# Kernel optimization log

Hardware: AMD Instinct MI355X
Metric: run time of the kernel (lower is better)

The kernel has to match this reference:

```python
import jax, jax.numpy as jnp
import numpy as np

J = 128
H = W = 1024
D = 2
NUM_CLS = 15
DEFAULT_SIGMA = 4096.0
TOPK = 0.95
LOSS_WEIGHT = 1.0
EPS = 1e-7


def setup_inputs() -> dict:
    key = jax.random.key(0)
    k1, k2, k3, k4 = jax.random.split(key, 4)
    mu = jax.random.uniform(k1, (J, 2), minval=0.0, maxval=float(H), dtype=jnp.float32)
    A = jax.random.normal(k2, (J, 2, 2), dtype=jnp.float32) * 8.0
    sigma = A @ A.transpose(0, 2, 1) + 100.0 * jnp.eye(2, dtype=jnp.float32)  # SPD covariances
    label = jax.random.randint(k3, (J,), 0, NUM_CLS)
    image = jax.random.normal(k4, (3, H, W), dtype=jnp.float32)
    pos_thres = jnp.full((16,), 0.3, jnp.float32)
    neg_thres = jnp.full((16,), 0.05, jnp.float32)
    return dict(mu=mu, sigma=sigma, label=label, image=image,
                pos_thres=pos_thres, neg_thres=neg_thres)


def _resize_bilinear_ac(x, Ho, Wo):
    # bilinear upsample with align_corners=True (matches F.interpolate)
    h, w = x.shape
    ry = jnp.arange(Ho, dtype=jnp.float32) * (h - 1) / (Ho - 1)
    rx = jnp.arange(Wo, dtype=jnp.float32) * (w - 1) / (Wo - 1)
    y0 = jnp.floor(ry).astype(jnp.int32); y1 = jnp.minimum(y0 + 1, h - 1); wy = ry - y0
    x0 = jnp.floor(rx).astype(jnp.int32); x1 = jnp.minimum(x0 + 1, w - 1); wx = rx - x0
    top = x[y0][:, x0] * (1 - wx)[None] + x[y0][:, x1] * wx[None]
    bot = x[y1][:, x0] * (1 - wx)[None] + x[y1][:, x1] * wx[None]
    return top * (1 - wy)[:, None] + bot * wy[:, None]


def _forward(mu, sigma, label, image, pos_thres, neg_thres):
    h, w = H // D, W // D
    # grid exactly like torch.linspace(0, h, h) + meshgrid(indexing='xy')
    x = jnp.linspace(0.0, h, h)
    y = jnp.linspace(0.0, w, w)
    X, Y = jnp.meshgrid(x, y, indexing='xy')  # [h, w] (h == w)
    mm = jnp.round(jax.lax.stop_gradient(mu) / D)  # [J, 2]

    # 'gaussian-orientation': keep eigenvectors, rescale eigenvalues to default area
    Ls, Vs = jnp.linalg.eigh(sigma)               # Ls [J,2], Vs [J,2,2]
    Ld = jax.lax.stop_gradient(Ls)
    Lsc = Ld / jnp.sqrt(Ld[:, 0:1] * Ld[:, 1:2]) * DEFAULT_SIGMA
    sg = jnp.einsum('jik,jk,jlk->jil', jax.lax.stop_gradient(Vs), Lsc,
                    jax.lax.stop_gradient(Vs)) / (D ** 2)  # [J,2,2]

    # analytic 2x2 inverse for the Mahalanobis form
    a, b, c = sg[:, 0, 0], sg[:, 0, 1], sg[:, 1, 1]
    det = a * c - b * b
    ia, ib, ic = c / det, -b / det, a / det
    dx = X[None] - mm[:, 0, None, None]  # [J,h,w]
    dy = Y[None] - mm[:, 1, None, None]
    maha = (ia[:, None, None] * dx * dx + 2 * ib[:, None, None] * dx * dy
            + ic[:, None, None] * dy * dy)
    g = jnp.exp(-0.5 * maha)             # [J,h,w] Gaussian Voronoi scores
    val = jnp.max(g, 0)
    vor = jnp.argmax(g, 0).astype(jnp.int32)

    # upsample: nearest (repeat) for labels, bilinear align_corners for values
    vor_full = jnp.repeat(jnp.repeat(vor, D, axis=0), D, axis=1)   # [H,W]
    val_full = _resize_bilinear_ac(val, H, W)                      # [H,W]

    cls = label[vor_full]

    # ridge detection: 3x3 Laplacian on the label map != 0
    kernel = jnp.ones((1, 1, 3, 3), jnp.float32).at[0, 0, 1, 1].set(-8.0)
    lap = jax.lax.conv_general_dilated(vor_full.astype(jnp.float32)[None, None],
                                       kernel, (1, 1), 'SAME')[0, 0]
    ridges = lap != 0

    vor1 = vor_full + 1
    vor1 = jnp.where(val_full < pos_thres[cls], 0, vor1)
    vor1 = jnp.where(val_full < neg_thres[cls], J + 1, vor1)
    vor1 = jnp.where(ridges, J + 1, vor1)
    # cv2.watershed on the CPU image is an external non-differentiable refinement;
    # the Voronoi markers are used directly as the watershed result here.
    markers = vor1  # [H,W], values in [0, J+1]

    # per-instance extent in the eigenbasis, via segment reductions over pixels
    gxx, gyy = jnp.meshgrid(jnp.arange(W, dtype=jnp.float32),
                            jnp.arange(H, dtype=jnp.float32), indexing='xy')
    pix = jnp.stack([gxx, gyy], -1).reshape(-1, 2)    # (x, y) per pixel
    seg = markers.reshape(-1)
    idx = jnp.clip(seg - 1, 0, J - 1)
    d = pix - mu[idx]                                 # [P,2]
    rot = jnp.einsum('pik,pi->pk', Vs[idx], d)        # V[j]^T (p - mu[j])
    m = jax.ops.segment_max(jnp.abs(rot), seg, num_segments=J + 2)  # [J+2,2]
    cnt = jax.ops.segment_sum(jnp.ones(seg.shape, jnp.float32), seg,
                              num_segments=J + 2)
    m_inst, c_inst = m[1:J + 1], cnt[1:J + 1]
    L_target = jnp.where(c_inst[:, None] > 0, m_inst ** 2, Ld)
    L_target = jax.lax.stop_gradient(L_target)        # .detach() in original

    # gwd_sigma_loss on diagonal Sigmas (diag_embed(L) vs diag_embed(L_target))
    Lp, Lt = Ls, L_target
    whr = Lp.sum(-1) + Lt.sum(-1)
    tr = (Lp * Lt).sum(-1)
    det_sqrt = jnp.sqrt(jnp.clip(Lp.prod(-1) * Lt.prod(-1), EPS))
    whr = whr - 2 * jnp.sqrt(jnp.clip(tr + 2 * det_sqrt, EPS))
    dist = jnp.sqrt(jnp.clip(whr, EPS))
    scale = 2 * jnp.clip(jnp.sqrt(jnp.clip(jnp.sqrt(jnp.clip(det_sqrt, EPS)), EPS)), EPS)
    dist = dist / scale
    loss_i = 1.0 - 1.0 / (1.0 + jnp.log1p(dist))      # fun='log1p', tau=1.0

    k = int(np.ceil(J * TOPK))
    smallest = -jax.lax.top_k(-loss_i, k)[0]
    return LOSS_WEIGHT * smallest.mean()


def reference(mu, sigma, label, image, pos_thres, neg_thres):
    return _forward(mu, sigma, label, image, pos_thres, neg_thres)
```

## Files before the change

kernel.cpp:

```cpp
#include <hip/hip_runtime.h>
#include <math.h>

#define NJ 128
#define HH 512
#define WW 512
#define FEPS 1e-7f
#define QT  32
#define THS (QT + 2)
#define TLP 36

__device__ __forceinline__ void eig2x2(float a, float b, float c,
                                       float& l0, float& l1,
                                       float& V00, float& V10, float& V01, float& V11) {
    float mean = 0.5f * (a + c);
    float diff = 0.5f * (a - c);
    float disc = sqrtf(diff * diff + b * b);
    l0 = mean - disc;
    l1 = mean + disc;
    float ux, uy;
    if (diff >= 0.f) { ux = diff + disc; uy = b; }
    else             { ux = b;           uy = disc - diff; }
    float nn = sqrtf(ux * ux + uy * uy);
    if (nn > 0.f) { ux /= nn; uy /= nn; } else { ux = 1.f; uy = 0.f; }
    V00 = -uy; V10 = ux;
    V01 =  ux; V11 = uy;
}

__global__ __launch_bounds__(256, 2) void k_vorf(
        const float* __restrict__ mu, const float* __restrict__ sigma,
        float* __restrict__ val, int* __restrict__ vor,
        unsigned* __restrict__ gml) {
    __shared__ float4 lp[NJ];
    __shared__ float  lic[NJ];
    int tid = threadIdx.x;
    if (tid < NJ) {
        int j = tid;
        float a = sigma[j * 4 + 0];
        float b = sigma[j * 4 + 1];
        float c = sigma[j * 4 + 3];
        float l0, l1, V00, V10, V01, V11;
        eig2x2(a, b, c, l0, l1, V00, V10, V01, V11);
        float gmean = sqrtf(l0 * l1);
        float lsc0 = l0 / gmean * 4096.f;
        float lsc1 = l1 / gmean * 4096.f;
        float s00 = (V00 * V00 * lsc0 + V01 * V01 * lsc1) * 0.25f;
        float s01 = (V00 * V10 * lsc0 + V01 * V11 * lsc1) * 0.25f;
        float s11 = (V10 * V10 * lsc0 + V11 * V11 * lsc1) * 0.25f;
        float det = s00 * s11 - s01 * s01;
        float4 q;
        q.x = rintf(mu[j * 2 + 0] * 0.5f);
        q.y = rintf(mu[j * 2 + 1] * 0.5f);
        q.z =  s11 / det;
        q.w = -2.f * s01 / det;
        lp[j]  = q;
        lic[j] = s00 / det;
    }
    if (blockIdx.x == 0 && tid < NJ) {
        gml[tid * 16 + 0] = 0u;
        gml[tid * 16 + 1] = 0u;
        gml[tid * 16 + 2] = 0u;
    }
    __syncthreads();

    int t = blockIdx.x * 256 + tid;
    int c = t & 511;
    int r = t >> 9;
    const float SCALE = 512.0f / 511.0f;
    float xc = (float)c * SCALE;
    float ya = (float)r * SCALE;
    float yb = (float)(r + 256) * SCALE;
    float bestA = 3.4e38f, bestB = 3.4e38f;
    int bjA = 0, bjB = 0;
    #pragma unroll 4
    for (int j = 0; j < NJ; ++j) {
        float4 p = lp[j];
        float ic = lic[j];
        float dx  = xc - p.x;
        float dyA = ya - p.y;
        float dyB = yb - p.y;
        float qA = p.z * dx * dx + p.w * dx * dyA + ic * dyA * dyA;
        float qB = p.z * dx * dx + p.w * dx * dyB + ic * dyB * dyB;
        if (qA < bestA) { bestA = qA; bjA = j; }
        if (qB < bestB) { bestB = qB; bjB = j; }
    }
    int pA = r * WW + c, pB = (r + 256) * WW + c;
    val[pA] = expf(-0.5f * bestA); vor[pA] = bjA;
    val[pB] = expf(-0.5f * bestB); vor[pB] = bjB;
}

__global__ __launch_bounds__(1024) void k_markt(
        const float* __restrict__ mu, const float* __restrict__ sigma,
        const int* __restrict__ label, const float* __restrict__ pos_thres,
        const float* __restrict__ neg_thres,
        const float* __restrict__ val, const int* __restrict__ vor,
        unsigned* __restrict__ gml) {
    __shared__ float4   lvv[NJ];
    __shared__ float2   lmu[NJ];
    __shared__ float    lpt[NJ], lnt[NJ];
    __shared__ float    tval[THS][TLP];
    __shared__ int      tvor[THS][TLP];
    __shared__ unsigned lm0[NJ], lm1[NJ];
    __shared__ int      lflag[NJ];

    int tid = threadIdx.x;
    if (tid < NJ) {
        int j = tid;
        float a = sigma[j * 4 + 0];
        float b = sigma[j * 4 + 1];
        float cc = sigma[j * 4 + 3];
        float l0, l1, V00, V10, V01, V11;
        eig2x2(a, b, cc, l0, l1, V00, V10, V01, V11);
        lvv[j] = make_float4(V00, V10, V01, V11);
        lmu[j] = make_float2(mu[j * 2 + 0], mu[j * 2 + 1]);
        int cl = label[j];
        lpt[j] = pos_thres[cl];
        lnt[j] = neg_thres[cl];
        lm0[j] = 0u; lm1[j] = 0u; lflag[j] = 0;
    }

    int A0 = (blockIdx.x >> 4) * QT;
    int B0 = (blockIdx.x & 15) * QT;

    for (int idx = tid; idx < THS * THS; idx += 1024) {
        int hu = idx / THS, hw = idx - hu * THS;
        int gy = A0 + hu - 1, gx = B0 + hw - 1;
        float vv = 0.f; int jv = 0;
        if (gy >= 0 && gy < HH && gx >= 0 && gx < WW) {
            int g = gy * WW + gx;
            vv = val[g]; jv = vor[g];
        }
        tval[hu][hw] = vv; tvor[hu][hw] = jv;
    }
    __syncthreads();

    int lane = tid & 63;
    {
        int u = tid >> 5;
        int v = tid & 31;
        int a = A0 + u, b = B0 + v;
        bool aM = a > 0, aP = a < 511, bM = b > 0, bP = b < 511;
        int hmm_ = (aM && bM) ? tvor[u    ][v    ] : 0;
        int hm0_ =  aM        ? tvor[u    ][v + 1] : 0;
        int hm1_ = (aM && bP) ? tvor[u    ][v + 2] : 0;
        int h0m_ =  bM        ? tvor[u + 1][v    ] : 0;
        int h00_ =              tvor[u + 1][v + 1];
        int h0p_ =  bP        ? tvor[u + 1][v + 2] : 0;
        int hpm_ = (aP && bM) ? tvor[u + 2][v    ] : 0;
        int hp0_ =  aP        ? tvor[u + 2][v + 1] : 0;
        int hpp_ = (aP && bP) ? tvor[u + 2][v + 2] : 0;
        int lap00 = -5 * h00_ + hmm_ + 2 * hm0_ + 2 * h0m_;
        int lap01 = -5 * h00_ + 2 * hm0_ + hm1_ + 2 * h0p_;
        int lap10 = -5 * h00_ + 2 * h0m_ + hpm_ + 2 * hp0_;
        int lap11 = -5 * h00_ + 2 * h0p_ + 2 * hp0_ + hpp_;
        int hv = h00_;
        float  pt = lpt[hv], nt = lnt[hv];
        float4 Vv = lvv[hv];
        float2 mv = lmu[hv];
        float m0 = -1.f, m1 = -1.f;

#define DO_PIXEL(U, V, LAP) {                                                  \
    int i = 2 * a + (U), jx = 2 * b + (V);                                     \
    float ry = ((float)i  * 511.0f) / 1023.0f;                                 \
    float rx = ((float)jx * 511.0f) / 1023.0f;                                 \
    int y0 = (int)ry; int y1 = min(y0 + 1, 511); float wy = ry - (float)y0;    \
    int x0 = (int)rx; int x1 = min(x0 + 1, 511); float wx = rx - (float)x0;    \
    int ly0 = y0 - A0 + 1, ly1 = y1 - A0 + 1;                                  \
    int lx0 = x0 - B0 + 1, lx1 = x1 - B0 + 1;                                  \
    float top = tval[ly0][lx0] * (1.f - wx) + tval[ly0][lx1] * wx;             \
    float bot = tval[ly1][lx0] * (1.f - wx) + tval[ly1][lx1] * wx;             \
    float vf  = top * (1.f - wy) + bot * wy;                                   \
    int mk = hv + 1;                                                           \
    if (vf < pt)     mk = 0;                                                   \
    if (vf < nt)     mk = NJ + 1;                                              \
    if ((LAP) != 0)  mk = NJ + 1;                                              \
    if (mk >= 1 && mk <= NJ) {                                                 \
        float dx = (float)jx - mv.x, dy = (float)i - mv.y;                     \
        float r0 = fabsf(Vv.x * dx + Vv.y * dy);                               \
        float r1 = fabsf(Vv.z * dx + Vv.w * dy);                               \
        m0 = fmaxf(m0, r0); m1 = fmaxf(m1, r1);                                \
    } }

        DO_PIXEL(0, 0, lap00)
        DO_PIXEL(0, 1, lap01)
        DO_PIXEL(1, 0, lap10)
        DO_PIXEL(1, 1, lap11)
#undef DO_PIXEL

        int inst = (m0 >= 0.f) ? hv : -1;
        #pragma unroll
        for (int d = 1; d < 64; d <<= 1) {
            int   oi = __shfl_up(inst, d);
            float o0 = __shfl_up(m0, d);
            float o1 = __shfl_up(m1, d);
            if (lane >= d && oi == inst) { m0 = fmaxf(m0, o0); m1 = fmaxf(m1, o1); }
        }
        int ni = __shfl_down(inst, 1);
        bool leader = (inst >= 0) && (lane == 63 || ni != inst);
        if (leader) {
            atomicMax(&lm0[inst], __float_as_uint(m0));
            atomicMax(&lm1[inst], __float_as_uint(m1));
            lflag[inst] = 1;
        }
    }
    __syncthreads();

    if (tid < NJ && lflag[tid]) {
        atomicMax(&gml[tid * 16 + 0], lm0[tid]);
        atomicMax(&gml[tid * 16 + 1], lm1[tid]);
        gml[tid * 16 + 2] = 1u;
    }
}

__global__ __launch_bounds__(128) void k_loss(
        const float* __restrict__ sigma, const unsigned* __restrict__ gml,
        float* __restrict__ out) {
    __shared__ float lb[NJ];
    __shared__ float wtot[2], wtop[2];
    int j = threadIdx.x;

    float aa = sigma[j * 4 + 0];
    float bb = sigma[j * 4 + 1];
    float cc = sigma[j * 4 + 3];
    float ls0, ls1, V00, V10, V01, V11;
    eig2x2(aa, bb, cc, ls0, ls1, V00, V10, V01, V11);
    float g0 = __uint_as_float(gml[j * 16 + 0]);
    float g1 = __uint_as_float(gml[j * 16 + 1]);
    bool has = gml[j * 16 + 2] > 0u;
    float lt0 = has ? g0 * g0 : ls0;
    float lt1 = has ? g1 * g1 : ls1;
    float whr = (ls0 + ls1) + (lt0 + lt1);
    float tr  = ls0 * lt0 + ls1 * lt1;
    float det_sqrt = sqrtf(fmaxf((ls0 * ls1) * (lt0 * lt1), FEPS));
    whr = whr - 2.f * sqrtf(fmaxf(tr + 2.f * det_sqrt, FEPS));
    float dist = sqrtf(fmaxf(whr, FEPS));
    float scale = 2.f * fmaxf(sqrtf(fmaxf(sqrtf(fmaxf(det_sqrt, FEPS)), FEPS)), FEPS);
    dist = dist / scale;
    float li = 1.f - 1.f / (1.f + log1pf(dist));
    lb[j] = li;
    __syncthreads();

    int rank = 0;
    #pragma unroll 8
    for (int t = 0; t < NJ; ++t) {
        float o = lb[t];
        rank += (o > li || (o == li && t < j)) ? 1 : 0;
    }
    float tot = li;
    float top = (rank < 6) ? li : 0.f;

    #pragma unroll
    for (int d = 32; d > 0; d >>= 1) {
        tot += __shfl_down(tot, d);
        top += __shfl_down(top, d);
    }
    if ((j & 63) == 0) { wtot[j >> 6] = tot; wtop[j >> 6] = top; }
    __syncthreads();
    if (j == 0)
        out[0] = 1.0f * ((wtot[0] + wtot[1]) - (wtop[0] + wtop[1])) / 122.f;
}

extern "C" void kernel_launch(void* const* d_in, const int* in_sizes, int n_in,
                              void* d_out, int out_size, void* d_ws, size_t ws_size,
                              hipStream_t stream) {
    const float* mu        = (const float*)d_in[0];
    const float* sigma     = (const float*)d_in[1];
    const int*   label     = (const int*)d_in[2];
    const float* pos_thres = (const float*)d_in[4];
    const float* neg_thres = (const float*)d_in[5];
    float* out = (float*)d_out;

    float*    val = (float*)d_ws;
    int*      vor = (int*)((char*)d_ws + (size_t)HH * WW * 4);
    unsigned* gml = (unsigned*)((char*)d_ws + 2ull * HH * WW * 4);

    k_vorf <<<(HH * WW / 2) / 256, 256, 0, stream>>>(mu, sigma, val, vor, gml);
    k_markt<<<256, 1024, 0, stream>>>(mu, sigma, label, pos_thres, neg_thres,
                                      val, vor, gml);
    k_loss <<<1, 128, 0, stream>>>(sigma, gml, out);
}
```

Before: 27.59 us.

## Fuse Voronoi assignment into mark kernel, recomputing halo tiles in shared memory

Merges the per-pixel nearest-Gaussian search into the tile kernel, so each block computes its own 34x34 halo tile straight into shared memory instead of reading it from a global val/vor buffer. This removes one kernel launch and the 2MB global write and read-back. In exchange, halo pixels are computed redundantly, about 13% extra work. Only 1156 of the 1024 threads' slots are used, so a few threads do two pixels and the 128-step loop sits on the critical path. Zeroing gml moves to a hipMemsetAsync, which adds a memset operation to the stream.

```diff
diff --git a/kernel.cpp b/kernel.cpp
--- a/kernel.cpp
+++ b/kernel.cpp
@@ -26,12 +26,21 @@
     V01 =  ux; V11 = uy;
 }
 
-__global__ __launch_bounds__(256, 2) void k_vorf(
+__global__ __launch_bounds__(1024) void k_fused(
         const float* __restrict__ mu, const float* __restrict__ sigma,
-        float* __restrict__ val, int* __restrict__ vor,
+        const int* __restrict__ label, const float* __restrict__ pos_thres,
+        const float* __restrict__ neg_thres,
         unsigned* __restrict__ gml) {
-    __shared__ float4 lp[NJ];
-    __shared__ float  lic[NJ];
+    __shared__ float4   lp[NJ];
+    __shared__ float    lic[NJ];
+    __shared__ float4   lvv[NJ];
+    __shared__ float2   lmu[NJ];
+    __shared__ float    lpt[NJ], lnt[NJ];
+    __shared__ float    tval[THS][TLP];
+    __shared__ int      tvor[THS][TLP];
+    __shared__ unsigned lm0[NJ], lm1[NJ];
+    __shared__ int      lflag[NJ];
+
     int tid = threadIdx.x;
     if (tid < NJ) {
         int j = tid;
@@ -54,62 +63,6 @@
         q.w = -2.f * s01 / det;
         lp[j]  = q;
         lic[j] = s00 / det;
-    }
-    if (blockIdx.x == 0 && tid < NJ) {
-        gml[tid * 16 + 0] = 0u;
-        gml[tid * 16 + 1] = 0u;
-        gml[tid * 16 + 2] = 0u;
-    }
-    __syncthreads();
-
-    int t = blockIdx.x * 256 + tid;
-    int c = t & 511;
-    int r = t >> 9;
-    const float SCALE = 512.0f / 511.0f;
-    float xc = (float)c * SCALE;
-    float ya = (float)r * SCALE;
-    float yb = (float)(r + 256) * SCALE;
-    float bestA = 3.4e38f, bestB = 3.4e38f;
-    int bjA = 0, bjB = 0;
-    #pragma unroll 4
-    for (int j = 0; j < NJ; ++j) {
-        float4 p = lp[j];
-        float ic = lic[j];
-        float dx  = xc - p.x;
-        float dyA = ya - p.y;
-        float dyB = yb - p.y;
-        float qA = p.z * dx * dx + p.w * dx * dyA + ic * dyA * dyA;
-        float qB = p.z * dx * dx + p.w * dx * dyB + ic * dyB * dyB;
-        if (qA < bestA) { bestA = qA; bjA = j; }
-        if (qB < bestB) { bestB = qB; bjB = j; }
-    }
-    int pA = r * WW + c, pB = (r + 256) * WW + c;
-    val[pA] = expf(-0.5f * bestA); vor[pA] = bjA;
-    val[pB] = expf(-0.5f * bestB); vor[pB] = bjB;
-}
-
-__global__ __launch_bounds__(1024) void k_markt(
-        const float* __restrict__ mu, const float* __restrict__ sigma,
-        const int* __restrict__ label, const float* __restrict__ pos_thres,
-        const float* __restrict__ neg_thres,
-        const float* __restrict__ val, const int* __restrict__ vor,
-        unsigned* __restrict__ gml) {
-    __shared__ float4   lvv[NJ];
-    __shared__ float2   lmu[NJ];
-    __shared__ float    lpt[NJ], lnt[NJ];
-    __shared__ float    tval[THS][TLP];
-    __shared__ int      tvor[THS][TLP];
-    __shared__ unsigned lm0[NJ], lm1[NJ];
-    __shared__ int      lflag[NJ];
-
-    int tid = threadIdx.x;
-    if (tid < NJ) {
-        int j = tid;
-        float a = sigma[j * 4 + 0];
-        float b = sigma[j * 4 + 1];
-        float cc = sigma[j * 4 + 3];
-        float l0, l1, V00, V10, V01, V11;
-        eig2x2(a, b, cc, l0, l1, V00, V10, V01, V11);
         lvv[j] = make_float4(V00, V10, V01, V11);
         lmu[j] = make_float2(mu[j * 2 + 0], mu[j * 2 + 1]);
         int cl = label[j];
@@ -117,19 +70,32 @@
         lnt[j] = neg_thres[cl];
         lm0[j] = 0u; lm1[j] = 0u; lflag[j] = 0;
     }
+    __syncthreads();
 
     int A0 = (blockIdx.x >> 4) * QT;
     int B0 = (blockIdx.x & 15) * QT;
 
+    const float SCALE = 512.0f / 511.0f;
     for (int idx = tid; idx < THS * THS; idx += 1024) {
         int hu = idx / THS, hw = idx - hu * THS;
-        int gy = A0 + hu - 1, gx = B0 + hw - 1;
-        float vv = 0.f; int jv = 0;
-        if (gy >= 0 && gy < HH && gx >= 0 && gx < WW) {
-            int g = gy * WW + gx;
-            vv = val[g]; jv = vor[g];
+        int ca = A0 + hu - 1, cb = B0 + hw - 1;
+        float vo = 0.f; int jo = 0;
+        if (ca >= 0 && ca < HH && cb >= 0 && cb < WW) {
+            float xc = (float)cb * SCALE;
+            float yr = (float)ca * SCALE;
+            float best = 3.4e38f; int bj = 0;
+            #pragma unroll 4
+            for (int j = 0; j < NJ; ++j) {
+                float4 p = lp[j];
+                float ic = lic[j];
+                float dx = xc - p.x;
+                float dy = yr - p.y;
+                float q = p.z * dx * dx + p.w * dx * dy + ic * dy * dy;
+                if (q < best) { best = q; bj = j; }
+            }
+            vo = expf(-0.5f * best); jo = bj;
         }
-        tval[hu][hw] = vv; tvor[hu][hw] = jv;
+        tval[hu][hw] = vo; tvor[hu][hw] = jo;
     }
     __syncthreads();
 
@@ -269,12 +235,9 @@
     const float* neg_thres = (const float*)d_in[5];
     float* out = (float*)d_out;
 
-    float*    val = (float*)d_ws;
-    int*      vor = (int*)((char*)d_ws + (size_t)HH * WW * 4);
-    unsigned* gml = (unsigned*)((char*)d_ws + 2ull * HH * WW * 4);
-
-    k_vorf <<<(HH * WW / 2) / 256, 256, 0, stream>>>(mu, sigma, val, vor, gml);
-    k_markt<<<256, 1024, 0, stream>>>(mu, sigma, label, pos_thres, neg_thres,
-                                      val, vor, gml);
+    unsigned* gml = (unsigned*)d_ws;
+
+    hipMemsetAsync(gml, 0, NJ * 16 * sizeof(unsigned), stream);
+    k_fused<<<256, 1024, 0, stream>>>(mu, sigma, label, pos_thres, neg_thres, gml);
     k_loss <<<1, 128, 0, stream>>>(sigma, gml, out);
 }
```

Result: slower. 31.79 us (+15.2%).

## Fuse loss kernel into markt via last-block atomic counter; interleave val/vor

Applied to the files above, without the earlier changes.

Removes the separate single-block loss kernel by having the last k_markt block, found through an atomic arrival counter, compute the per-instance GWD loss and top-k mean. The Voronoi value and index arrays are also packed into one float2 array, so each halo element needs a single load. This saves one kernel launch plus the gap between launches, at the cost of a global atomic per block and atomic reads of gml to see other blocks' results.

```diff
diff --git a/kernel.cpp b/kernel.cpp
--- a/kernel.cpp
+++ b/kernel.cpp
@@ -28,8 +28,8 @@
 
 __global__ __launch_bounds__(256, 2) void k_vorf(
         const float* __restrict__ mu, const float* __restrict__ sigma,
-        float* __restrict__ val, int* __restrict__ vor,
-        unsigned* __restrict__ gml) {
+        float2* __restrict__ vv, unsigned* __restrict__ gml,
+        unsigned* __restrict__ bar) {
     __shared__ float4 lp[NJ];
     __shared__ float  lic[NJ];
     int tid = threadIdx.x;
@@ -59,6 +59,7 @@
         gml[tid * 16 + 0] = 0u;
         gml[tid * 16 + 1] = 0u;
         gml[tid * 16 + 2] = 0u;
+        if (tid == 0) *bar = 0u;
     }
     __syncthreads();
 
@@ -83,17 +84,19 @@
         if (qA < bestA) { bestA = qA; bjA = j; }
         if (qB < bestB) { bestB = qB; bjB = j; }
     }
-    int pA = r * WW + c, pB = (r + 256) * WW + c;
-    val[pA] = expf(-0.5f * bestA); vor[pA] = bjA;
-    val[pB] = expf(-0.5f * bestB); vor[pB] = bjB;
+    float2 wA; wA.x = expf(-0.5f * bestA); wA.y = __int_as_float(bjA);
+    float2 wB; wB.x = expf(-0.5f * bestB); wB.y = __int_as_float(bjB);
+    vv[r * WW + c] = wA;
+    vv[(r + 256) * WW + c] = wB;
 }
 
 __global__ __launch_bounds__(1024) void k_markt(
         const float* __restrict__ mu, const float* __restrict__ sigma,
         const int* __restrict__ label, const float* __restrict__ pos_thres,
         const float* __restrict__ neg_thres,
-        const float* __restrict__ val, const int* __restrict__ vor,
-        unsigned* __restrict__ gml) {
+        const float2* __restrict__ vv,
+        unsigned* __restrict__ gml, unsigned* __restrict__ bar,
+        float* __restrict__ out) {
     __shared__ float4   lvv[NJ];
     __shared__ float2   lmu[NJ];
     __shared__ float    lpt[NJ], lnt[NJ];
@@ -101,6 +104,9 @@
     __shared__ int      tvor[THS][TLP];
     __shared__ unsigned lm0[NJ], lm1[NJ];
     __shared__ int      lflag[NJ];
+    __shared__ float    lb[NJ];
+    __shared__ float    wtot[2], wtop[2];
+    __shared__ int      isLast;
 
     int tid = threadIdx.x;
     if (tid < NJ) {
@@ -124,12 +130,12 @@
     for (int idx = tid; idx < THS * THS; idx += 1024) {
         int hu = idx / THS, hw = idx - hu * THS;
         int gy = A0 + hu - 1, gx = B0 + hw - 1;
-        float vv = 0.f; int jv = 0;
+        float v0 = 0.f; int j0 = 0;
         if (gy >= 0 && gy < HH && gx >= 0 && gx < WW) {
-            int g = gy * WW + gx;
-            vv = val[g]; jv = vor[g];
-        }
-        tval[hu][hw] = vv; tvor[hu][hw] = jv;
+            float2 tv = vv[gy * WW + gx];
+            v0 = tv.x; j0 = __float_as_int(tv.y);
+        }
+        tval[hu][hw] = v0; tvor[hu][hw] = j0;
     }
     __syncthreads();
 
@@ -207,55 +213,58 @@
     if (tid < NJ && lflag[tid]) {
         atomicMax(&gml[tid * 16 + 0], lm0[tid]);
         atomicMax(&gml[tid * 16 + 1], lm1[tid]);
-        gml[tid * 16 + 2] = 1u;
-    }
-}
-
-__global__ __launch_bounds__(128) void k_loss(
-        const float* __restrict__ sigma, const unsigned* __restrict__ gml,
-        float* __restrict__ out) {
-    __shared__ float lb[NJ];
-    __shared__ float wtot[2], wtop[2];
-    int j = threadIdx.x;
-
-    float aa = sigma[j * 4 + 0];
-    float bb = sigma[j * 4 + 1];
-    float cc = sigma[j * 4 + 3];
-    float ls0, ls1, V00, V10, V01, V11;
-    eig2x2(aa, bb, cc, ls0, ls1, V00, V10, V01, V11);
-    float g0 = __uint_as_float(gml[j * 16 + 0]);
-    float g1 = __uint_as_float(gml[j * 16 + 1]);
-    bool has = gml[j * 16 + 2] > 0u;
-    float lt0 = has ? g0 * g0 : ls0;
-    float lt1 = has ? g1 * g1 : ls1;
-    float whr = (ls0 + ls1) + (lt0 + lt1);
-    float tr  = ls0 * lt0 + ls1 * lt1;
-    float det_sqrt = sqrtf(fmaxf((ls0 * ls1) * (lt0 * lt1), FEPS));
-    whr = whr - 2.f * sqrtf(fmaxf(tr + 2.f * det_sqrt, FEPS));
-    float dist = sqrtf(fmaxf(whr, FEPS));
-    float scale = 2.f * fmaxf(sqrtf(fmaxf(sqrtf(fmaxf(det_sqrt, FEPS)), FEPS)), FEPS);
-    dist = dist / scale;
-    float li = 1.f - 1.f / (1.f + log1pf(dist));
-    lb[j] = li;
-    __syncthreads();
-
-    int rank = 0;
-    #pragma unroll 8
-    for (int t = 0; t < NJ; ++t) {
-        float o = lb[t];
-        rank += (o > li || (o == li && t < j)) ? 1 : 0;
-    }
-    float tot = li;
-    float top = (rank < 6) ? li : 0.f;
-
-    #pragma unroll
-    for (int d = 32; d > 0; d >>= 1) {
-        tot += __shfl_down(tot, d);
-        top += __shfl_down(top, d);
-    }
-    if ((j & 63) == 0) { wtot[j >> 6] = tot; wtop[j >> 6] = top; }
-    __syncthreads();
-    if (j == 0)
+        atomicOr (&gml[tid * 16 + 2], 1u);
+    }
+
+    __syncthreads();
+    if (tid == 0) {
+        unsigned done = atomicAdd(bar, 1u);
+        isLast = (done == gridDim.x - 1) ? 1 : 0;
+    }
+    __syncthreads();
+    if (!isLast) return;
+
+    float li = 0.f;
+    if (tid < NJ) {
+        float aa = sigma[tid * 4 + 0];
+        float bb = sigma[tid * 4 + 1];
+        float cc = sigma[tid * 4 + 3];
+        float ls0, ls1, V00, V10, V01, V11;
+        eig2x2(aa, bb, cc, ls0, ls1, V00, V10, V01, V11);
+        float g0 = __uint_as_float(atomicMax(&gml[tid * 16 + 0], 0u));
+        float g1 = __uint_as_float(atomicMax(&gml[tid * 16 + 1], 0u));
+        unsigned has = atomicAdd(&gml[tid * 16 + 2], 0u);
+        float lt0 = has ? g0 * g0 : ls0;
+        float lt1 = has ? g1 * g1 : ls1;
+        float whr = (ls0 + ls1) + (lt0 + lt1);
+        float tr  = ls0 * lt0 + ls1 * lt1;
+        float det_sqrt = sqrtf(fmaxf((ls0 * ls1) * (lt0 * lt1), FEPS));
+        whr = whr - 2.f * sqrtf(fmaxf(tr + 2.f * det_sqrt, FEPS));
+        float dist = sqrtf(fmaxf(whr, FEPS));
+        float scale = 2.f * fmaxf(sqrtf(fmaxf(sqrtf(fmaxf(det_sqrt, FEPS)), FEPS)), FEPS);
+        dist = dist / scale;
+        li = 1.f - 1.f / (1.f + log1pf(dist));
+        lb[tid] = li;
+    }
+    __syncthreads();
+    if (tid < NJ) {
+        int rank = 0;
+        #pragma unroll 8
+        for (int t = 0; t < NJ; ++t) {
+            float o = lb[t];
+            rank += (o > li || (o == li && t < tid)) ? 1 : 0;
+        }
+        float tot = li;
+        float top = (rank < 6) ? li : 0.f;
+        #pragma unroll
+        for (int d = 32; d > 0; d >>= 1) {
+            tot += __shfl_down(tot, d);
+            top += __shfl_down(top, d);
+        }
+        if ((tid & 63) == 0) { wtot[tid >> 6] = tot; wtop[tid >> 6] = top; }
+    }
+    __syncthreads();
+    if (tid == 0)
         out[0] = 1.0f * ((wtot[0] + wtot[1]) - (wtop[0] + wtop[1])) / 122.f;
 }
 
@@ -269,12 +278,11 @@
     const float* neg_thres = (const float*)d_in[5];
     float* out = (float*)d_out;
 
-    float*    val = (float*)d_ws;
-    int*      vor = (int*)((char*)d_ws + (size_t)HH * WW * 4);
+    float2*   vv  = (float2*)d_ws;
     unsigned* gml = (unsigned*)((char*)d_ws + 2ull * HH * WW * 4);
-
-    k_vorf <<<(HH * WW / 2) / 256, 256, 0, stream>>>(mu, sigma, val, vor, gml);
+    unsigned* bar = gml + NJ * 16;
+
+    k_vorf <<<(HH * WW / 2) / 256, 256, 0, stream>>>(mu, sigma, vv, gml, bar);
     k_markt<<<256, 1024, 0, stream>>>(mu, sigma, label, pos_thres, neg_thres,
-                                      val, vor, gml);
-    k_loss <<<1, 128, 0, stream>>>(sigma, gml, out);
-}
+                                      vv, gml, bar, out);
+}
```

Result: slower. 28.60 us (+3.7%).
